# Optimization experiments

Hardware: AMD Instinct MI355X
Metric: run time of the kernel (lower is better)

## Reference

```python
import jax, jax.numpy as jnp
import numpy as np

B, T, F, U = 256, 512, 64, 128

def setup_inputs() -> dict:
    key = jax.random.key(0)
    ks = jax.random.split(key, 8)
    def ortho(k, n):
        a = jax.random.normal(k, (n, n), dtype=jnp.float32)
        q, _ = jnp.linalg.qr(a)
        return q.astype(jnp.float32)
    return {
        "x": jax.random.normal(ks[0], (B, T, F), dtype=jnp.float32),
        "m": jax.random.uniform(ks[1], (B, T, F), dtype=jnp.float32),
        "delta_t": jax.random.uniform(ks[2], (B, T), dtype=jnp.float32),
        "W_z": jax.random.normal(ks[3], (F, U), dtype=jnp.float32) * 0.08,
        "U_z": ortho(ks[4], U),
        "b_z": jnp.zeros((U,), jnp.float32),
        "W_r": jax.random.normal(ks[5], (F, U), dtype=jnp.float32) * 0.08,
        "U_r": ortho(ks[6], U),
        "b_r": jnp.zeros((U,), jnp.float32),
        "W_h": jax.random.normal(ks[7], (F, U), dtype=jnp.float32) * 0.08,
        "U_h": ortho(jax.random.fold_in(key, 99), U),
        "b_h": jnp.zeros((U,), jnp.float32),
        "gamma_x_decay": jnp.ones((F,), jnp.float32),
        "gamma_h_decay": jnp.ones((U,), jnp.float32),
        "mean_imputation": jnp.zeros((F,), jnp.float32),
    }

def reference(x, m, delta_t, W_z, U_z, b_z, W_r, U_r, b_r, W_h, U_h, b_h,
              gamma_x_decay, gamma_h_decay, mean_imputation):
    # delta_t: [B,T] -> [B,T,1]
    dt = delta_t[..., None]
    # input-side decay + imputation (no recurrence -> fully vectorized)
    gamma_x = jnp.exp(-jnp.maximum(0.0, gamma_x_decay) * dt)          # [B,T,F]
    x_dec = m * x + (1.0 - m) * (gamma_x * x + (1.0 - gamma_x) * mean_imputation)
    gamma_h = jnp.exp(-jnp.maximum(0.0, gamma_h_decay) * dt)          # [B,T,U]
    # precompute input projections for all timesteps
    xz = jnp.einsum('btf,fu->btu', x_dec, W_z) + b_z
    xr = jnp.einsum('btf,fu->btu', x_dec, W_r) + b_r
    xh = jnp.einsum('btf,fu->btu', x_dec, W_h) + b_h

    def step(h, inp):
        gz, az, ar, ah = inp            # gamma_h_t [B,U], projected inputs [B,U]
        h_dec = gz * h
        z = jax.nn.sigmoid(az + h_dec @ U_z)
        r = jax.nn.sigmoid(ar + h_dec @ U_r)
        h_hat = jnp.tanh(ah + (r * h_dec) @ U_h)
        h_new = (1.0 - z) * h_dec + z * h_hat
        return h_new, h_new

    h0 = jnp.zeros((x.shape[0], U_z.shape[0]), x.dtype)
    xs = (jnp.swapaxes(gamma_h, 0, 1), jnp.swapaxes(xz, 0, 1),
          jnp.swapaxes(xr, 0, 1), jnp.swapaxes(xh, 0, 1))
    _, hs = jax.lax.scan(step, h0, xs)  # [T,B,U]
    return jnp.swapaxes(hs, 0, 1)       # [B,T,U]
```

## Files before the change

### kernel.cpp

```cpp
#include <hip/hip_runtime.h>

#define B_ 256
#define T_ 512
#define F_ 64
#define U_ 128

typedef _Float16 h2v __attribute__((ext_vector_type(2)));
union U32H2 { unsigned u; h2v h; };

__device__ __forceinline__ float fdot2(unsigned a, unsigned b, float c) {
  U32H2 x, y; x.u = a; y.u = b;
  return __builtin_amdgcn_fdot2(x.h, y.h, c, false);
}
__device__ __forceinline__ unsigned packh2(float a, float b) {
  U32H2 r; r.h[0] = (_Float16)a; r.h[1] = (_Float16)b; return r.u;
}
__device__ __forceinline__ float pairsum(float v) {
  int t = __builtin_amdgcn_update_dpp(0, __float_as_int(v), 0xB1, 0xF, 0xF, true);
  return v + __int_as_float(t);
}
__device__ __forceinline__ float fast_sig(float x) {
  return __builtin_amdgcn_rcpf(1.0f + __expf(-x));
}
__device__ __forceinline__ float fast_tanh(float x) {
  return fmaf(-2.0f, __builtin_amdgcn_rcpf(1.0f + __expf(2.0f * x)), 1.0f);
}

#define D4(acc, Hv, Wr, o)                                        \
  acc = fdot2(Hv.x, Wr[(o)], acc);                                \
  acc = fdot2(Hv.y, Wr[(o) + 1], acc);                            \
  acc = fdot2(Hv.z, Wr[(o) + 2], acc);                            \
  acc = fdot2(Hv.w, Wr[(o) + 3], acc);

__global__ __launch_bounds__(256, 1)
__attribute__((amdgpu_waves_per_eu(1, 1)))
void grud_kernel(
    const float* __restrict__ x, const float* __restrict__ m,
    const float* __restrict__ delta_t,
    const float* __restrict__ Wz_, const float* __restrict__ Uz, const float* __restrict__ bz,
    const float* __restrict__ Wr_, const float* __restrict__ Ur, const float* __restrict__ br,
    const float* __restrict__ Wh_, const float* __restrict__ Uh, const float* __restrict__ bh,
    const float* __restrict__ gxd, const float* __restrict__ ghd,
    const float* __restrict__ mi,
    float* __restrict__ out)
{
  const int tid = threadIdx.x;
  const int b   = blockIdx.x;
  const int w   = tid >> 6;
  const int l   = tid & 63;
  const int c   = 32 * w + (l >> 1);
  const int p   = l & 1;
  const bool ev = (p == 0);

  __shared__ float  s_dt[520];
  __shared__ float  s_ghv[32 * U_];
  __shared__ float  s_hist[32 * U_];
  __shared__ __align__(16) ushort s_x16[32 * F_];
  __shared__ __align__(16) ushort s_hd16[U_];
  __shared__ __align__(16) ushort s_rh16[U_];
  __shared__ float  s_negg[U_];
  __shared__ float  s_gxf[F_];
  __shared__ float  s_mi[F_];

  unsigned uz[32], ur[32], uh[32];
  unsigned wz[16], wr[16], wh[16];
#pragma unroll
  for (int j = 0; j < 32; ++j) {
    const int k0 = 64 * p + 2 * j;
    uz[j] = packh2(Uz[k0 * U_ + c], Uz[(k0 + 1) * U_ + c]);
    ur[j] = packh2(Ur[k0 * U_ + c], Ur[(k0 + 1) * U_ + c]);
    uh[j] = packh2(Uh[k0 * U_ + c], Uh[(k0 + 1) * U_ + c]);
  }
#pragma unroll
  for (int j = 0; j < 16; ++j) {
    const int f0 = 32 * p + 2 * j;
    wz[j] = packh2(Wz_[f0 * U_ + c], Wz_[(f0 + 1) * U_ + c]);
    wr[j] = packh2(Wr_[f0 * U_ + c], Wr_[(f0 + 1) * U_ + c]);
    wh[j] = packh2(Wh_[f0 * U_ + c], Wh_[(f0 + 1) * U_ + c]);
  }
  const float bzc = bz[c], brc = br[c], bhc = bh[c];

  {
    const float* dtb = delta_t + (size_t)b * T_;
    s_dt[tid]       = dtb[tid];
    s_dt[tid + 256] = dtb[tid + 256];
    if (tid < 8)   s_dt[512 + tid] = 0.0f;
    if (tid < U_)  { s_negg[tid] = -fmaxf(ghd[tid], 0.0f); ((unsigned*)s_hd16)[tid >> 1] = 0u; }
    if (tid < F_)  { s_gxf[tid] = -fmaxf(gxd[tid], 0.0f); s_mi[tid] = mi[tid]; }
  }
  __syncthreads();

  float hd_own = 0.0f;
  float axz = 0.f, axr = 0.f, axh = 0.f;

  for (int t0 = 0; t0 < T_; t0 += 32) {
#pragma unroll
    for (int i = 0; i < 2; ++i) {
      const int e4 = tid + 256 * i;
      const int t = e4 >> 4, f0 = (e4 & 15) << 2;
      const float dtv = s_dt[t0 + t];
      const float4 xv  = *(const float4*)(x + (size_t)(b * T_ + t0 + t) * F_ + f0);
      const float4 mv  = *(const float4*)(m + (size_t)(b * T_ + t0 + t) * F_ + f0);
      const float4 gv  = *(const float4*)(s_gxf + f0);
      const float4 miv = *(const float4*)(s_mi + f0);
      float gx, d0, d1, d2, d3;
      gx = __expf(gv.x * dtv);
      d0 = fmaf(mv.x, xv.x, (1.0f - mv.x) * (gx * xv.x + (1.0f - gx) * miv.x));
      gx = __expf(gv.y * dtv);
      d1 = fmaf(mv.y, xv.y, (1.0f - mv.y) * (gx * xv.y + (1.0f - gx) * miv.y));
      gx = __expf(gv.z * dtv);
      d2 = fmaf(mv.z, xv.z, (1.0f - mv.z) * (gx * xv.z + (1.0f - gx) * miv.z));
      gx = __expf(gv.w * dtv);
      d3 = fmaf(mv.w, xv.w, (1.0f - mv.w) * (gx * xv.w + (1.0f - gx) * miv.w));
      uint2 px; px.x = packh2(d0, d1); px.y = packh2(d2, d3);
      *(uint2*)(s_x16 + 4 * e4) = px;
    }
#pragma unroll
    for (int i = 0; i < 16; ++i) {
      const int e = tid + 256 * i;
      const int t = e >> 7, cc = e & 127;
      s_ghv[e] = __expf(s_negg[cc] * s_dt[t0 + t + 1]);
    }
    __syncthreads();

    {
      const uint4* xp = (const uint4*)(s_x16 + 32 * p);
      float a0 = 0.f, a1 = 0.f, a2 = 0.f;
#pragma unroll
      for (int q = 0; q < 4; ++q) {
        const uint4 Xv = xp[q];
        D4(a0, Xv, wz, 4 * q) D4(a1, Xv, wr, 4 * q) D4(a2, Xv, wh, 4 * q)
      }
      axz = a0; axr = a1; axh = a2;
    }

#pragma unroll 1
    for (int tc = 0; tc < 32; ++tc) {
      float az0 = axz, az1 = 0.f, ar0 = axr, ar1 = 0.f;
      {
        const uint4* hp = (const uint4*)(s_hd16 + 64 * p);
#pragma unroll
        for (int jj = 0; jj < 4; ++jj) {
          const uint4 Ha = hp[jj], Hb = hp[jj + 4];
          D4(az0, Ha, uz, 4 * jj)  D4(az1, Hb, uz, 4 * jj + 16)
          D4(ar0, Ha, ur, 4 * jj)  D4(ar1, Hb, ur, 4 * jj + 16)
        }
      }
      const float az = pairsum(az0 + az1) + bzc;
      const float ar = pairsum(ar0 + ar1) + brc;
      const float z = fast_sig(az);
      const float r = fast_sig(ar);
      if (ev) ((_Float16*)s_rh16)[c] = (_Float16)(r * hd_own);
      __syncthreads();

      float ah0 = axh, ah1 = 0.f;
      {
        const uint4* rp = (const uint4*)(s_rh16 + 64 * p);
#pragma unroll
        for (int jj = 0; jj < 4; ++jj) {
          const uint4 Ra = rp[jj], Rb = rp[jj + 4];
          D4(ah0, Ra, uh, 4 * jj)  D4(ah1, Rb, uh, 4 * jj + 16)
        }
      }
      if (tc < 31) {
        const uint4* xp = (const uint4*)(s_x16 + (tc + 1) * F_ + 32 * p);
        float a0 = 0.f, a1 = 0.f, a2 = 0.f;
#pragma unroll
        for (int q = 0; q < 4; ++q) {
          const uint4 Xv = xp[q];
          D4(a0, Xv, wz, 4 * q) D4(a1, Xv, wr, 4 * q) D4(a2, Xv, wh, 4 * q)
        }
        axz = a0; axr = a1; axh = a2;
      }
      const float ah = pairsum(ah0 + ah1) + bhc;
      const float hh = fast_tanh(ah);
      const float hn = fmaf(z, hh - hd_own, hd_own);
      if (ev) s_hist[tc * U_ + c] = hn;
      hd_own = s_ghv[tc * U_ + c] * hn;
      if (ev) ((_Float16*)s_hd16)[c] = (_Float16)hd_own;
      __syncthreads();
    }

    {
      const float4* h4 = (const float4*)s_hist;
      float4* o4 = (float4*)(out + (size_t)(b * T_ + t0) * U_);
#pragma unroll
      for (int i = 0; i < 4; ++i) o4[tid + 256 * i] = h4[tid + 256 * i];
    }
  }
}

extern "C" void kernel_launch(void* const* d_in, const int* in_sizes, int n_in,
                              void* d_out, int out_size, void* d_ws, size_t ws_size,
                              hipStream_t stream) {
  const float* x   = (const float*)d_in[0];
  const float* m   = (const float*)d_in[1];
  const float* dt  = (const float*)d_in[2];
  const float* Wz  = (const float*)d_in[3];
  const float* Uz  = (const float*)d_in[4];
  const float* bz  = (const float*)d_in[5];
  const float* Wr  = (const float*)d_in[6];
  const float* Ur  = (const float*)d_in[7];
  const float* br  = (const float*)d_in[8];
  const float* Wh  = (const float*)d_in[9];
  const float* Uh  = (const float*)d_in[10];
  const float* bh  = (const float*)d_in[11];
  const float* gxd = (const float*)d_in[12];
  const float* ghd = (const float*)d_in[13];
  const float* mi  = (const float*)d_in[14];

  grud_kernel<<<dim3(B_), dim3(256), 0, stream>>>(
      x, m, dt, Wz, Uz, bz, Wr, Ur, br, Wh, Uh, bh, gxd, ghd, mi, (float*)d_out);
}
```

Before: 365.1 us.

## Split z/r gates across lane pairs and precompute chunk input projections

Each lane pair now splits work by gate instead of by K half. The even lane computes the full z dot product and the odd lane the full r dot product, which removes the cross-lane reductions for those gates. Input projections for a 32-step chunk are computed up front into shared memory instead of being interleaved into the recurrent loop. The gamma_h decay is computed on the fly from a small delta_t buffer. Hidden-state history is kept as fp16 in shared memory, reused as the x staging buffer, and widened back to fp32 when written out, which adds rounding error to the outputs.

```diff
diff --git a/kernel.cpp b/kernel.cpp
--- a/kernel.cpp
+++ b/kernel.cpp
@@ -15,9 +15,12 @@
 __device__ __forceinline__ unsigned packh2(float a, float b) {
   U32H2 r; r.h[0] = (_Float16)a; r.h[1] = (_Float16)b; return r.u;
 }
+__device__ __forceinline__ float pairswap(float v) {
+  return __int_as_float(
+      __builtin_amdgcn_update_dpp(0, __float_as_int(v), 0xB1, 0xF, 0xF, true));
+}
 __device__ __forceinline__ float pairsum(float v) {
-  int t = __builtin_amdgcn_update_dpp(0, __float_as_int(v), 0xB1, 0xF, 0xF, true);
-  return v + __int_as_float(t);
+  return v + pairswap(v);
 }
 __device__ __forceinline__ float fast_sig(float x) {
   return __builtin_amdgcn_rcpf(1.0f + __expf(-x));
@@ -46,59 +49,75 @@
 {
   const int tid = threadIdx.x;
   const int b   = blockIdx.x;
-  const int w   = tid >> 6;
-  const int l   = tid & 63;
-  const int c   = 32 * w + (l >> 1);
-  const int p   = l & 1;
-  const bool ev = (p == 0);
-
-  __shared__ float  s_dt[520];
-  __shared__ float  s_ghv[32 * U_];
-  __shared__ float  s_hist[32 * U_];
-  __shared__ __align__(16) ushort s_x16[32 * F_];
+  const int c   = tid >> 1;
+  const int p   = tid & 1;
+  const bool p0 = (p == 0);
+
+  __shared__ float  s_ax[3 * 32 * U_];
+  __shared__ __align__(16) ushort s_hist16[32 * U_];
+  __shared__ float  s_dt[40];
+  __shared__ float  s_gxf[F_], s_mi[F_];
   __shared__ __align__(16) ushort s_hd16[U_];
   __shared__ __align__(16) ushort s_rh16[U_];
-  __shared__ float  s_negg[U_];
-  __shared__ float  s_gxf[F_];
-  __shared__ float  s_mi[F_];
-
-  unsigned uz[32], ur[32], uh[32];
+  ushort* const s_x16 = s_hist16;
+
+  unsigned uf[64];
+  unsigned uh[32];
   unsigned wz[16], wr[16], wh[16];
-#pragma unroll
-  for (int j = 0; j < 32; ++j) {
-    const int k0 = 64 * p + 2 * j;
-    uz[j] = packh2(Uz[k0 * U_ + c], Uz[(k0 + 1) * U_ + c]);
-    ur[j] = packh2(Ur[k0 * U_ + c], Ur[(k0 + 1) * U_ + c]);
-    uh[j] = packh2(Uh[k0 * U_ + c], Uh[(k0 + 1) * U_ + c]);
+  {
+    const float* Ucol = p0 ? Uz : Ur;
+#pragma unroll
+    for (int j = 0; j < 64; ++j)
+      uf[j] = packh2(Ucol[(2 * j) * U_ + c], Ucol[(2 * j + 1) * U_ + c]);
+#pragma unroll
+    for (int j = 0; j < 32; ++j) {
+      const int k0 = 64 * p + 2 * j;
+      uh[j] = packh2(Uh[k0 * U_ + c], Uh[(k0 + 1) * U_ + c]);
+    }
+#pragma unroll
+    for (int j = 0; j < 16; ++j) {
+      const int f0 = 32 * p + 2 * j;
+      wz[j] = packh2(Wz_[f0 * U_ + c], Wz_[(f0 + 1) * U_ + c]);
+      wr[j] = packh2(Wr_[f0 * U_ + c], Wr_[(f0 + 1) * U_ + c]);
+      wh[j] = packh2(Wh_[f0 * U_ + c], Wh_[(f0 + 1) * U_ + c]);
+    }
   }
-#pragma unroll
-  for (int j = 0; j < 16; ++j) {
-    const int f0 = 32 * p + 2 * j;
-    wz[j] = packh2(Wz_[f0 * U_ + c], Wz_[(f0 + 1) * U_ + c]);
-    wr[j] = packh2(Wr_[f0 * U_ + c], Wr_[(f0 + 1) * U_ + c]);
-    wh[j] = packh2(Wh_[f0 * U_ + c], Wh_[(f0 + 1) * U_ + c]);
-  }
-  const float bzc = bz[c], brc = br[c], bhc = bh[c];
-
-  {
-    const float* dtb = delta_t + (size_t)b * T_;
-    s_dt[tid]       = dtb[tid];
-    s_dt[tid + 256] = dtb[tid + 256];
-    if (tid < 8)   s_dt[512 + tid] = 0.0f;
-    if (tid < U_)  { s_negg[tid] = -fmaxf(ghd[tid], 0.0f); ((unsigned*)s_hd16)[tid >> 1] = 0u; }
-    if (tid < F_)  { s_gxf[tid] = -fmaxf(gxd[tid], 0.0f); s_mi[tid] = mi[tid]; }
-  }
+  const float bz_c = p0 ? bz[c] : 0.0f;
+  const float bh_c = p0 ? bh[c] : 0.0f;
+  const float br_c = p0 ? 0.0f  : br[c];
+  const float negg = p0 ? 0.0f  : -fmaxf(ghd[c], 0.0f);
+
+  if (tid < F_) { s_gxf[tid] = -fmaxf(gxd[tid], 0.0f); s_mi[tid] = mi[tid]; }
+  if (tid < 64) ((unsigned*)s_hd16)[tid] = 0u;
   __syncthreads();
 
   float hd_own = 0.0f;
-  float axz = 0.f, axr = 0.f, axh = 0.f;
+  float zreg   = 0.0f;
 
   for (int t0 = 0; t0 < T_; t0 += 32) {
+    if (t0 > 0) {
+      const uint4 ha = *(const uint4*)(s_hist16 + 16 * tid);
+      const uint4 hb = *(const uint4*)(s_hist16 + 16 * tid + 8);
+      float* ob = out + (size_t)(b * T_ + (t0 - 32)) * U_ + 16 * tid;
+      const unsigned wa[8] = {ha.x, ha.y, ha.z, ha.w, hb.x, hb.y, hb.z, hb.w};
+#pragma unroll
+      for (int i = 0; i < 8; ++i) {
+        U32H2 u; u.u = wa[i];
+        ob[2 * i]     = (float)u.h[0];
+        ob[2 * i + 1] = (float)u.h[1];
+      }
+      __syncthreads();
+    }
+
+    if (tid < 33) {
+      const int t = t0 + tid;
+      s_dt[tid] = (t < T_) ? delta_t[b * T_ + t] : 0.0f;
+    }
 #pragma unroll
     for (int i = 0; i < 2; ++i) {
       const int e4 = tid + 256 * i;
       const int t = e4 >> 4, f0 = (e4 & 15) << 2;
-      const float dtv = s_dt[t0 + t];
+      const float dtv = delta_t[b * T_ + t0 + t];
       const float4 xv  = *(const float4*)(x + (size_t)(b * T_ + t0 + t) * F_ + f0);
       const float4 mv  = *(const float4*)(m + (size_t)(b * T_ + t0 + t) * F_ + f0);
       const float4 gv  = *(const float4*)(s_gxf + f0);
@@ -115,77 +134,77 @@
       uint2 px; px.x = packh2(d0, d1); px.y = packh2(d2, d3);
       *(uint2*)(s_x16 + 4 * e4) = px;
     }
-#pragma unroll
-    for (int i = 0; i < 16; ++i) {
-      const int e = tid + 256 * i;
-      const int t = e >> 7, cc = e & 127;
-      s_ghv[e] = __expf(s_negg[cc] * s_dt[t0 + t + 1]);
-    }
     __syncthreads();
 
-    {
-      const uint4* xp = (const uint4*)(s_x16 + 32 * p);
+#pragma unroll 2
+    for (int t = 0; t < 32; ++t) {
+      const uint4* xp = (const uint4*)(s_x16 + t * F_ + 32 * p);
       float a0 = 0.f, a1 = 0.f, a2 = 0.f;
 #pragma unroll
       for (int q = 0; q < 4; ++q) {
         const uint4 Xv = xp[q];
         D4(a0, Xv, wz, 4 * q) D4(a1, Xv, wr, 4 * q) D4(a2, Xv, wh, 4 * q)
       }
-      axz = a0; axr = a1; axh = a2;
-    }
-
-#pragma unroll 1
+      a0 = pairsum(a0); a1 = pairsum(a1); a2 = pairsum(a2);
+      if (p0) {
+        s_ax[t * U_ + c]            = a0 + bz_c;
+        s_ax[2 * 4096 + t * U_ + c] = a2 + bh_c;
+      } else {
+        s_ax[4096 + t * U_ + c]     = a1 + br_c;
+      }
+    }
+    __syncthreads();
+
+#pragma unroll 2
     for (int tc = 0; tc < 32; ++tc) {
-      float az0 = axz, az1 = 0.f, ar0 = axr, ar1 = 0.f;
-      {
-        const uint4* hp = (const uint4*)(s_hd16 + 64 * p);
-#pragma unroll
-        for (int jj = 0; jj < 4; ++jj) {
-          const uint4 Ha = hp[jj], Hb = hp[jj + 4];
-          D4(az0, Ha, uz, 4 * jj)  D4(az1, Hb, uz, 4 * jj + 16)
-          D4(ar0, Ha, ur, 4 * jj)  D4(ar1, Hb, ur, 4 * jj + 16)
-        }
-      }
-      const float az = pairsum(az0 + az1) + bzc;
-      const float ar = pairsum(ar0 + ar1) + brc;
-      const float z = fast_sig(az);
-      const float r = fast_sig(ar);
-      if (ev) ((_Float16*)s_rh16)[c] = (_Float16)(r * hd_own);
+      const float axg = s_ax[p * 4096 + tc * U_ + c];
+      const uint4* hp = (const uint4*)s_hd16;
+      float a0 = 0.f, a1 = 0.f, a2 = 0.f, a3 = 0.f;
+#pragma unroll
+      for (int q = 0; q < 4; ++q) {
+        const uint4 Ha = hp[4 * q + 0], Hb = hp[4 * q + 1];
+        const uint4 Hc = hp[4 * q + 2], Hd = hp[4 * q + 3];
+        D4(a0, Ha, uf, 16 * q)      D4(a1, Hb, uf, 16 * q + 4)
+        D4(a2, Hc, uf, 16 * q + 8)  D4(a3, Hd, uf, 16 * q + 12)
+      }
+      const float g = fast_sig(((a0 + a1) + (a2 + a3)) + axg);
+      if (p0) zreg = g;
+      else    ((_Float16*)s_rh16)[c] = (_Float16)(g * hd_own);
       __syncthreads();
 
-      float ah0 = axh, ah1 = 0.f;
-      {
-        const uint4* rp = (const uint4*)(s_rh16 + 64 * p);
-#pragma unroll
-        for (int jj = 0; jj < 4; ++jj) {
-          const uint4 Ra = rp[jj], Rb = rp[jj + 4];
-          D4(ah0, Ra, uh, 4 * jj)  D4(ah1, Rb, uh, 4 * jj + 16)
-        }
-      }
-      if (tc < 31) {
-        const uint4* xp = (const uint4*)(s_x16 + (tc + 1) * F_ + 32 * p);
-        float a0 = 0.f, a1 = 0.f, a2 = 0.f;
-#pragma unroll
-        for (int q = 0; q < 4; ++q) {
-          const uint4 Xv = xp[q];
-          D4(a0, Xv, wz, 4 * q) D4(a1, Xv, wr, 4 * q) D4(a2, Xv, wh, 4 * q)
-        }
-        axz = a0; axr = a1; axh = a2;
-      }
-      const float ah = pairsum(ah0 + ah1) + bhc;
+      const float axh = s_ax[2 * 4096 + tc * U_ + c];
+      float gh = 0.0f;
+      if (!p0) gh = __expf(negg * s_dt[tc + 1]);
+      const uint4* rp = (const uint4*)(s_rh16 + 64 * p);
+      float h0 = 0.f, h1 = 0.f;
+#pragma unroll
+      for (int q = 0; q < 4; ++q) {
+        const uint4 Ra = rp[q], Rb = rp[q + 4];
+        D4(h0, Ra, uh, 4 * q)  D4(h1, Rb, uh, 4 * q + 16)
+      }
+      const float ah = pairsum(h0 + h1) + axh;
       const float hh = fast_tanh(ah);
-      const float hn = fmaf(z, hh - hd_own, hd_own);
-      if (ev) s_hist[tc * U_ + c] = hn;
-      hd_own = s_ghv[tc * U_ + c] * hn;
-      if (ev) ((_Float16*)s_hd16)[c] = (_Float16)hd_own;
+      const float gh_sw = pairswap(gh);
+      const float hn = fmaf(zreg, hh - hd_own, hd_own);
+      if (p0) ((_Float16*)s_hist16)[tc * U_ + c] = (_Float16)hn;
+      const float hdn = gh_sw * hn;
+      const float hdn_sw = pairswap(hdn);
+      hd_own = p0 ? hdn : hdn_sw;
+      if (p0) ((_Float16*)s_hd16)[c] = (_Float16)hd_own;
       __syncthreads();
     }
-
-    {
-      const float4* h4 = (const float4*)s_hist;
-      float4* o4 = (float4*)(out + (size_t)(b * T_ + t0) * U_);
-#pragma unroll
-      for (int i = 0; i < 4; ++i) o4[tid + 256 * i] = h4[tid + 256 * i];
+  }
+
+  {
+    const uint4 ha = *(const uint4*)(s_hist16 + 16 * tid);
+    const uint4 hb = *(const uint4*)(s_hist16 + 16 * tid + 8);
+    float* ob = out + (size_t)(b * T_ + (T_ - 32)) * U_ + 16 * tid;
+    const unsigned wa[8] = {ha.x, ha.y, ha.z, ha.w, hb.x, hb.y, hb.z, hb.w};
+#pragma unroll
+    for (int i = 0; i < 8; ++i) {
+      U32H2 u; u.u = wa[i];
+      ob[2 * i]     = (float)u.h[0];
+      ob[2 * i + 1] = (float)u.h[1];
     }
   }
 }
```

After: 451.0 us. +23.5%, slower.

## Split recurrent dot products four ways per lane over two output columns

Applied to the files above, without the earlier changes.

Changes the thread-to-work mapping in the recurrent loop. Each group of four lanes now splits the K dimension four ways and computes two adjacent output columns, where before each pair of lanes split K two ways for a single column. The partial sums are combined with a two-stage DPP reduction, and h, r*h and the history are written as packed pairs, so shared-memory stores and reads of h are vectorized and the per-lane vector of h read per step is half as long. The cost is an extra DPP stage on the critical path plus more live accumulators per lane.

```diff
diff --git a/kernel.cpp b/kernel.cpp
--- a/kernel.cpp
+++ b/kernel.cpp
@@ -15,9 +15,12 @@
 __device__ __forceinline__ unsigned packh2(float a, float b) {
   U32H2 r; r.h[0] = (_Float16)a; r.h[1] = (_Float16)b; return r.u;
 }
-__device__ __forceinline__ float pairsum(float v) {
+__device__ __forceinline__ float red4(float v) {
   int t = __builtin_amdgcn_update_dpp(0, __float_as_int(v), 0xB1, 0xF, 0xF, true);
-  return v + __int_as_float(t);
+  v += __int_as_float(t);
+  t = __builtin_amdgcn_update_dpp(0, __float_as_int(v), 0x4E, 0xF, 0xF, true);
+  v += __int_as_float(t);
+  return v;
 }
 __device__ __forceinline__ float fast_sig(float x) {
   return __builtin_amdgcn_rcpf(1.0f + __expf(-x));
@@ -46,11 +49,10 @@
 {
   const int tid = threadIdx.x;
   const int b   = blockIdx.x;
-  const int w   = tid >> 6;
-  const int l   = tid & 63;
-  const int c   = 32 * w + (l >> 1);
-  const int p   = l & 1;
-  const bool ev = (p == 0);
+  const int kg  = tid & 3;
+  const int cp  = tid >> 2;
+  const int c0  = 2 * cp;
+  const bool wr_lane = (kg == 0);
 
   __shared__ float  s_dt[520];
   __shared__ float  s_ghv[32 * U_];
@@ -65,20 +67,28 @@
   unsigned uz[32], ur[32], uh[32];
   unsigned wz[16], wr[16], wh[16];
 #pragma unroll
-  for (int j = 0; j < 32; ++j) {
-    const int k0 = 64 * p + 2 * j;
-    uz[j] = packh2(Uz[k0 * U_ + c], Uz[(k0 + 1) * U_ + c]);
-    ur[j] = packh2(Ur[k0 * U_ + c], Ur[(k0 + 1) * U_ + c]);
-    uh[j] = packh2(Uh[k0 * U_ + c], Uh[(k0 + 1) * U_ + c]);
-  }
-#pragma unroll
   for (int j = 0; j < 16; ++j) {
-    const int f0 = 32 * p + 2 * j;
-    wz[j] = packh2(Wz_[f0 * U_ + c], Wz_[(f0 + 1) * U_ + c]);
-    wr[j] = packh2(Wr_[f0 * U_ + c], Wr_[(f0 + 1) * U_ + c]);
-    wh[j] = packh2(Wh_[f0 * U_ + c], Wh_[(f0 + 1) * U_ + c]);
-  }
-  const float bzc = bz[c], brc = br[c], bhc = bh[c];
+    const int k0 = 32 * kg + 2 * j;
+    uz[j]      = packh2(Uz[k0 * U_ + c0],     Uz[(k0 + 1) * U_ + c0]);
+    uz[16 + j] = packh2(Uz[k0 * U_ + c0 + 1], Uz[(k0 + 1) * U_ + c0 + 1]);
+    ur[j]      = packh2(Ur[k0 * U_ + c0],     Ur[(k0 + 1) * U_ + c0]);
+    ur[16 + j] = packh2(Ur[k0 * U_ + c0 + 1], Ur[(k0 + 1) * U_ + c0 + 1]);
+    uh[j]      = packh2(Uh[k0 * U_ + c0],     Uh[(k0 + 1) * U_ + c0]);
+    uh[16 + j] = packh2(Uh[k0 * U_ + c0 + 1], Uh[(k0 + 1) * U_ + c0 + 1]);
+  }
+#pragma unroll
+  for (int j = 0; j < 8; ++j) {
+    const int f0 = 16 * kg + 2 * j;
+    wz[j]     = packh2(Wz_[f0 * U_ + c0],     Wz_[(f0 + 1) * U_ + c0]);
+    wz[8 + j] = packh2(Wz_[f0 * U_ + c0 + 1], Wz_[(f0 + 1) * U_ + c0 + 1]);
+    wr[j]     = packh2(Wr_[f0 * U_ + c0],     Wr_[(f0 + 1) * U_ + c0]);
+    wr[8 + j] = packh2(Wr_[f0 * U_ + c0 + 1], Wr_[(f0 + 1) * U_ + c0 + 1]);
+    wh[j]     = packh2(Wh_[f0 * U_ + c0],     Wh_[(f0 + 1) * U_ + c0]);
+    wh[8 + j] = packh2(Wh_[f0 * U_ + c0 + 1], Wh_[(f0 + 1) * U_ + c0 + 1]);
+  }
+  const float bz0 = bz[c0], bz1 = bz[c0 + 1];
+  const float br0 = br[c0], br1 = br[c0 + 1];
+  const float bh0 = bh[c0], bh1 = bh[c0 + 1];
 
   {
     const float* dtb = delta_t + (size_t)b * T_;
@@ -90,8 +100,8 @@
   }
   __syncthreads();
 
-  float hd_own = 0.0f;
-  float axz = 0.f, axr = 0.f, axh = 0.f;
+  float hd0 = 0.0f, hd1 = 0.0f;
+  float axz0 = 0.f, axz1 = 0.f, axr0 = 0.f, axr1 = 0.f, axh0 = 0.f, axh1 = 0.f;
 
   for (int t0 = 0; t0 < T_; t0 += 32) {
 #pragma unroll
@@ -124,60 +134,65 @@
     __syncthreads();
 
     {
-      const uint4* xp = (const uint4*)(s_x16 + 32 * p);
-      float a0 = 0.f, a1 = 0.f, a2 = 0.f;
-#pragma unroll
-      for (int q = 0; q < 4; ++q) {
+      const uint4* xp = (const uint4*)(s_x16 + 16 * kg);
+      float a0 = 0.f, a1 = 0.f, a2 = 0.f, a3 = 0.f, a4 = 0.f, a5 = 0.f;
+#pragma unroll
+      for (int q = 0; q < 2; ++q) {
         const uint4 Xv = xp[q];
-        D4(a0, Xv, wz, 4 * q) D4(a1, Xv, wr, 4 * q) D4(a2, Xv, wh, 4 * q)
-      }
-      axz = a0; axr = a1; axh = a2;
+        D4(a0, Xv, wz, 4 * q)  D4(a1, Xv, wz, 8 + 4 * q)
+        D4(a2, Xv, wr, 4 * q)  D4(a3, Xv, wr, 8 + 4 * q)
+        D4(a4, Xv, wh, 4 * q)  D4(a5, Xv, wh, 8 + 4 * q)
+      }
+      axz0 = a0; axz1 = a1; axr0 = a2; axr1 = a3; axh0 = a4; axh1 = a5;
     }
 
 #pragma unroll 1
     for (int tc = 0; tc < 32; ++tc) {
-      float az0 = axz, az1 = 0.f, ar0 = axr, ar1 = 0.f;
-      {
-        const uint4* hp = (const uint4*)(s_hd16 + 64 * p);
-#pragma unroll
-        for (int jj = 0; jj < 4; ++jj) {
-          const uint4 Ha = hp[jj], Hb = hp[jj + 4];
-          D4(az0, Ha, uz, 4 * jj)  D4(az1, Hb, uz, 4 * jj + 16)
-          D4(ar0, Ha, ur, 4 * jj)  D4(ar1, Hb, ur, 4 * jj + 16)
+      const uint4* hp = (const uint4*)(s_hd16 + 32 * kg);
+      float az0 = axz0, az1 = axz1, ar0 = axr0, ar1 = axr1;
+#pragma unroll
+      for (int j = 0; j < 4; ++j) {
+        const uint4 Hv = hp[j];
+        D4(az0, Hv, uz, 4 * j)  D4(az1, Hv, uz, 16 + 4 * j)
+        D4(ar0, Hv, ur, 4 * j)  D4(ar1, Hv, ur, 16 + 4 * j)
+      }
+      const float z0 = fast_sig(red4(az0) + bz0);
+      const float z1 = fast_sig(red4(az1) + bz1);
+      const float r0 = fast_sig(red4(ar0) + br0);
+      const float r1 = fast_sig(red4(ar1) + br1);
+      if (wr_lane) ((unsigned*)s_rh16)[cp] = packh2(r0 * hd0, r1 * hd1);
+      __syncthreads();
+
+      const float2 ghv = ((const float2*)s_ghv)[tc * 64 + cp];
+      const uint4* rp = (const uint4*)(s_rh16 + 32 * kg);
+      float ah0 = axh0, ah1 = axh1;
+#pragma unroll
+      for (int j = 0; j < 4; ++j) {
+        const uint4 Rv = rp[j];
+        D4(ah0, Rv, uh, 4 * j)  D4(ah1, Rv, uh, 16 + 4 * j)
+      }
+      if (tc < 31) {
+        const uint4* xp = (const uint4*)(s_x16 + (tc + 1) * F_ + 16 * kg);
+        float a0 = 0.f, a1 = 0.f, a2 = 0.f, a3 = 0.f, a4 = 0.f, a5 = 0.f;
+#pragma unroll
+        for (int q = 0; q < 2; ++q) {
+          const uint4 Xv = xp[q];
+          D4(a0, Xv, wz, 4 * q)  D4(a1, Xv, wz, 8 + 4 * q)
+          D4(a2, Xv, wr, 4 * q)  D4(a3, Xv, wr, 8 + 4 * q)
+          D4(a4, Xv, wh, 4 * q)  D4(a5, Xv, wh, 8 + 4 * q)
         }
-      }
-      const float az = pairsum(az0 + az1) + bzc;
-      const float ar = pairsum(ar0 + ar1) + brc;
-      const float z = fast_sig(az);
-      const float r = fast_sig(ar);
-      if (ev) ((_Float16*)s_rh16)[c] = (_Float16)(r * hd_own);
-      __syncthreads();
-
-      float ah0 = axh, ah1 = 0.f;
-      {
-        const uint4* rp = (const uint4*)(s_rh16 + 64 * p);
-#pragma unroll
-        for (int jj = 0; jj < 4; ++jj) {
-          const uint4 Ra = rp[jj], Rb = rp[jj + 4];
-          D4(ah0, Ra, uh, 4 * jj)  D4(ah1, Rb, uh, 4 * jj + 16)
-        }
-      }
-      if (tc < 31) {
-        const uint4* xp = (const uint4*)(s_x16 + (tc + 1) * F_ + 32 * p);
-        float a0 = 0.f, a1 = 0.f, a2 = 0.f;
-#pragma unroll
-        for (int q = 0; q < 4; ++q) {
-          const uint4 Xv = xp[q];
-          D4(a0, Xv, wz, 4 * q) D4(a1, Xv, wr, 4 * q) D4(a2, Xv, wh, 4 * q)
-        }
-        axz = a0; axr = a1; axh = a2;
-      }
-      const float ah = pairsum(ah0 + ah1) + bhc;
-      const float hh = fast_tanh(ah);
-      const float hn = fmaf(z, hh - hd_own, hd_own);
-      if (ev) s_hist[tc * U_ + c] = hn;
-      hd_own = s_ghv[tc * U_ + c] * hn;
-      if (ev) ((_Float16*)s_hd16)[c] = (_Float16)hd_own;
+        axz0 = a0; axz1 = a1; axr0 = a2; axr1 = a3; axh0 = a4; axh1 = a5;
+      }
+      const float hh0 = fast_tanh(red4(ah0) + bh0);
+      const float hh1 = fast_tanh(red4(ah1) + bh1);
+      const float hn0 = fmaf(z0, hh0 - hd0, hd0);
+      const float hn1 = fmaf(z1, hh1 - hd1, hd1);
+      hd0 = ghv.x * hn0;
+      hd1 = ghv.y * hn1;
+      if (wr_lane) {
+        ((float2*)s_hist)[tc * 64 + cp] = make_float2(hn0, hn1);
+        ((unsigned*)s_hd16)[cp] = packh2(hd0, hd1);
+      }
       __syncthreads();
     }
 
```

Result: faster. 356.4 us (-2.4%).
